# Kernel optimization log

Hardware: AMD Instinct MI355X
Metric: run time of the kernel (lower is better)

Reference implementation:

```python
import jax, jax.numpy as jnp
import numpy as np

T, D = 2048, 2048
H, DN, DR, DV = 16, 128, 64, 128
QL, KVL = 768, 512
HI, DI, TOPK = 16, 128, 256
E, TKE, MI = 8, 2, 1024
EPS = 1e-6
RSF = 2.5
SCALE = (DN + DR) ** -0.5
NEG = jnp.float32(-1e30)


def rms_norm(x, w):
    xf = x.astype(jnp.float32)
    y = xf * jax.lax.rsqrt(jnp.mean(xf * xf, axis=-1, keepdims=True) + EPS)
    return (y * w).astype(x.dtype)


def layer_norm(x, w, b):
    xf = x.astype(jnp.float32)
    mu = jnp.mean(xf, axis=-1, keepdims=True)
    var = jnp.mean((xf - mu) ** 2, axis=-1, keepdims=True)
    return (((xf - mu) * jax.lax.rsqrt(var + EPS)) * w + b).astype(x.dtype)


def rope(x, pos):
    # neox-style half rotation; x: (T, ..., d)
    d = x.shape[-1]
    inv = 1.0 / (10000.0 ** (jnp.arange(0, d, 2, dtype=jnp.float32) / d))
    f = pos.astype(jnp.float32)[:, None] * inv  # (T, d/2)
    shp = (x.shape[0],) + (1,) * (x.ndim - 2) + (d // 2,)
    cos, sin = jnp.cos(f).reshape(shp), jnp.sin(f).reshape(shp)
    x1, x2 = jnp.split(x.astype(jnp.float32), 2, axis=-1)
    return jnp.concatenate([x1 * cos - x2 * sin, x2 * cos + x1 * sin], -1).astype(x.dtype)


def swiglu(x, w1, w3, w2):
    return (jax.nn.silu(x @ w1) * (x @ w3)) @ w2


def setup_inputs():
    key = jax.random.key(0)
    ks = iter(jax.random.split(key, 32))
    n = lambda shape, s=0.02: jax.random.normal(next(ks), shape, jnp.float32) * s
    return dict(
        positions=jnp.arange(T, dtype=jnp.int32),
        hidden_states=jax.random.normal(next(ks), (T, D), jnp.float32),
        w_in=jnp.ones((D,), jnp.float32),
        w_post=jnp.ones((D,), jnp.float32),
        W_qkv_a=n((D, QL + KVL + DR)),
        w_qa=jnp.ones((QL,), jnp.float32),
        w_kva=jnp.ones((KVL,), jnp.float32),
        W_qb=n((QL, H * (DN + DR))),
        W_ik=n((D, DI)),
        ik_ln_w=jnp.ones((DI,), jnp.float32),
        ik_ln_b=jnp.zeros((DI,), jnp.float32),
        W_iw=n((D, HI)),
        W_iqb=n((QL, HI * DI)),
        W_UKT=n((H, DN, KVL)),
        W_UV=n((H, KVL, DV)),
        W_o=n((H * DV, D)),
        W_gate=n((D, E)),
        We1=n((E, D, MI)), We3=n((E, D, MI)), We2=n((E, MI, D)),
        Ws1=n((D, MI)), Ws3=n((D, MI)), Ws2=n((MI, D)),
    )


def reference(positions, hidden_states, w_in, w_post, W_qkv_a, w_qa, w_kva, W_qb,
              W_ik, ik_ln_w, ik_ln_b, W_iw, W_iqb, W_UKT, W_UV, W_o, W_gate,
              We1, We3, We2, Ws1, Ws3, Ws2):
    # --- input norm (residual is None path) ---
    residual = hidden_states
    h = rms_norm(hidden_states, w_in)

    # --- fused qkv_a projection + split ---
    qkv = h @ W_qkv_a
    q_c, kv_c, k_pe = jnp.split(qkv, [QL, QL + KVL], axis=-1)

    # --- lightning indexer projections ---
    index_k = layer_norm(h @ W_ik, ik_ln_w, ik_ln_b)  # (T, DI)
    index_w = (h @ W_iw) * (HI ** -0.5)               # (T, HI)

    # --- fused_norm_rope: q_a/kv_a RMSNorm, RoPE on k_pe and index_k ---
    q_c = rms_norm(q_c, w_qa)
    kv_c = rms_norm(kv_c, w_kva)
    k_pe = rope(k_pe, positions)
    index_k = rope(index_k, positions)

    # --- q_b / indexer q projections + fused_q RoPE ---
    q = (q_c @ W_qb).reshape(T, H, DN + DR)
    q_nope, q_pe = q[..., :DN], rope(q[..., DN:], positions)
    index_q = rope((q_c @ W_iqb).reshape(T, HI, DI), positions) * (DI ** -0.5)

    # --- sparse_attn_indexer: weighted ReLU dot-product logits, causal top-k ---
    il = jnp.einsum('thd,sd->ths', index_q, index_k)
    il = jnp.einsum('ths,th->ts', jax.nn.relu(il), index_w)  # (T, T)
    causal = positions[:, None] >= positions[None, :]
    il = jnp.where(causal, il, NEG)
    topk_idx = jax.lax.top_k(il, TOPK)[1]  # (T, TOPK)
    mask = jnp.zeros((T, T), bool).at[jnp.arange(T)[:, None], topk_idx].set(True) & causal

    # --- MLA sparse decode (MQA in latent space) ---
    ql_nope = jnp.einsum('thd,hdk->thk', q_nope, W_UKT)       # (T, H, KVL)
    q_full = jnp.concatenate([ql_nope, q_pe], axis=-1)        # (T, H, KVL+DR)
    kv = jnp.concatenate([kv_c, k_pe], axis=-1)               # (T, KVL+DR)
    scores = jnp.einsum('thd,sd->ths', q_full, kv) * SCALE
    scores = jnp.where(mask[:, None, :], scores, NEG)
    attn = jax.nn.softmax(scores, axis=-1)
    ctx = jnp.einsum('ths,sk->thk', attn, kv_c)               # (T, H, KVL)
    o = jnp.einsum('thk,hkv->thv', ctx, W_UV).reshape(T, H * DV) @ W_o

    # --- add + post-attention norm ---
    residual = o + residual
    h = rms_norm(residual, w_post)

    # --- MoE: top-2 softmax routing over 8 experts + shared expert ---
    probs = jax.nn.softmax(h @ W_gate, axis=-1)
    tv, ti = jax.lax.top_k(probs, TKE)
    tw = tv / jnp.sum(tv, axis=-1, keepdims=True)
    routed = jnp.zeros_like(h)
    for e in range(E):
        we = jnp.sum(jnp.where(ti == e, tw, 0.0), axis=-1)  # (T,)
        routed = routed + we[:, None] * swiglu(h, We1[e], We3[e], We2[e])
    shared = swiglu(h, Ws1, Ws3, Ws2)
    # scale_and_add in fp32
    out = (routed.astype(jnp.float32) * RSF + shared.astype(jnp.float32)).astype(h.dtype)
    return out, residual
```

## Files before the change

kernel.cpp:

```cpp
#include <hip/hip_runtime.h>
#include <hip/hip_bf16.h>
#include <math.h>

#define TT 2048
#define DD 2048
#define NH 16
#define DNN 128
#define DRR 64
#define DVV 128
#define QLL 768
#define KVLL 512
#define HII 16
#define DII 128
#define TOPKN 256
#define NEE 8
#define MII 1024
#define QKVW 1488
#define QW 5120
#define EPSF 1e-6f
#define NEGF (-1e30f)
#define SCALEF 0.07216878364870323f
#define IQSCALE 0.08838834764831845f
#define LOG1E4 9.210340371976184f
#define CHK 512

typedef unsigned short u16;
typedef __attribute__((ext_vector_type(8))) short s8v;
typedef __attribute__((ext_vector_type(4))) float f4v;

__device__ inline void split_bf16(float x, u16& h, u16& l) {
  __hip_bfloat16 bh_ = __float2bfloat16(x);
  float hf = __bfloat162float(bh_);
  __hip_bfloat16 bl_ = __float2bfloat16(x - hf);
  h = *(u16*)&bh_; l = *(u16*)&bl_;
}
__device__ inline u16 rnd_bf16(float x) {
  __hip_bfloat16 b = __float2bfloat16(x);
  return *(u16*)&b;
}
__device__ inline float b2f(u16 h) { return __uint_as_float(((unsigned)h) << 16); }

__global__ __launch_bounds__(256) void rms_kernel(
    const float* __restrict__ src, int sstride, int width,
    const float* __restrict__ w,
    float* __restrict__ dstf, int dfstride,
    u16* __restrict__ dsthi, u16* __restrict__ dstlo, int dhstride)
{
  int t = blockIdx.x, tid = threadIdx.x;
  const float* x = src + (size_t)t * sstride;
  float ss = 0.f;
  for (int i = tid; i < width; i += 256) { float v = x[i]; ss += v * v; }
  for (int off = 32; off; off >>= 1) ss += __shfl_down(ss, off, 64);
  __shared__ float red[4];
  __shared__ float scale_sh;
  if ((tid & 63) == 0) red[tid >> 6] = ss;
  __syncthreads();
  if (tid == 0) {
    float tot = red[0] + red[1] + red[2] + red[3];
    scale_sh = rsqrtf(tot / (float)width + EPSF);
  }
  __syncthreads();
  float sc2 = scale_sh;
  for (int i = tid; i < width; i += 256) {
    float y = x[i] * sc2 * w[i];
    if (dstf) dstf[(size_t)t * dfstride + i] = y;
    if (dsthi) {
      if (dstlo) {
        u16 h, l; split_bf16(y, h, l);
        dsthi[(size_t)t * dhstride + i] = h;
        dstlo[(size_t)t * dhstride + i] = l;
      } else {
        dsthi[(size_t)t * dhstride + i] = rnd_bf16(y);
      }
    }
  }
}

__global__ __launch_bounds__(256) void res_rms(
    const float* __restrict__ o, const float* __restrict__ hid,
    const float* __restrict__ w,
    float* __restrict__ resid, u16* __restrict__ dhi, u16* __restrict__ dlo)
{
  int t = blockIdx.x, tid = threadIdx.x;
  long base = (long)t * DD;
  float xv[8];
  float ss = 0.f;
#pragma unroll
  for (int j = 0; j < 8; ++j) {
    int i = j * 256 + tid;
    float v = o[base + i] + hid[base + i];
    xv[j] = v; resid[base + i] = v; ss += v * v;
  }
  for (int off = 32; off; off >>= 1) ss += __shfl_down(ss, off, 64);
  __shared__ float red[4];
  __shared__ float scale_sh;
  if ((tid & 63) == 0) red[tid >> 6] = ss;
  __syncthreads();
  if (tid == 0) scale_sh = rsqrtf((red[0] + red[1] + red[2] + red[3]) / (float)DD + EPSF);
  __syncthreads();
  float sc2 = scale_sh;
#pragma unroll
  for (int j = 0; j < 8; ++j) {
    int i = j * 256 + tid;
    float y = xv[j] * sc2 * w[i];
    u16 h, l; split_bf16(y, h, l);
    dhi[base + i] = h; dlo[base + i] = l;
  }
}

__global__ __launch_bounds__(128) void ln_rope_ik(
    const float* __restrict__ src, int sstride,
    const float* __restrict__ w, const float* __restrict__ b,
    const int* __restrict__ pos, u16* __restrict__ dhi, u16* __restrict__ dlo)
{
  int t = blockIdx.x, tid = threadIdx.x;
  __shared__ float rowv[128];
  __shared__ float red[2];
  float v = src[(size_t)t * sstride + tid];
  float s = v;
  for (int off = 32; off; off >>= 1) s += __shfl_down(s, off, 64);
  if ((tid & 63) == 0) red[tid >> 6] = s;
  __syncthreads();
  float mu = (red[0] + red[1]) * (1.f / 128.f);
  __syncthreads();
  float dlt = v - mu;
  float s2 = dlt * dlt;
  for (int off = 32; off; off >>= 1) s2 += __shfl_down(s2, off, 64);
  if ((tid & 63) == 0) red[tid >> 6] = s2;
  __syncthreads();
  float var = (red[0] + red[1]) * (1.f / 128.f);
  float yv = dlt * rsqrtf(var + EPSF) * w[tid] + b[tid];
  rowv[tid] = yv;
  __syncthreads();
  if (tid < 64) {
    float x1 = rowv[tid], x2 = rowv[tid + 64];
    float p = (float)pos[t];
    float invf = expf(-(2.f * tid / 128.f) * LOG1E4);
    float f = p * invf;
    float cf = cosf(f), sf = sinf(f);
    float y1 = x1 * cf - x2 * sf;
    float y2 = x2 * cf + x1 * sf;
    u16 h1, l1, h2, l2;
    split_bf16(y1, h1, l1); split_bf16(y2, h2, l2);
    long base = (size_t)t * DII + tid;
    dhi[base] = h1; dlo[base] = l1;
    dhi[base + 64] = h2; dlo[base + 64] = l2;
  }
}

__global__ void rope_kpe(const float* __restrict__ qkv, const int* __restrict__ pos, u16* __restrict__ kvb)
{
  int t = blockIdx.x, tid = threadIdx.x;
  if (tid < 32) {
    const float* x = qkv + (size_t)t * QKVW + QLL + KVLL;
    float x1 = x[tid], x2 = x[tid + 32];
    float p = (float)pos[t];
    float invf = expf(-(2.f * tid / 64.f) * LOG1E4);
    float f = p * invf, cf = cosf(f), sf = sinf(f);
    kvb[(long)t * 576 + 512 + tid]      = rnd_bf16(x1 * cf - x2 * sf);
    kvb[(long)t * 576 + 512 + tid + 32] = rnd_bf16(x2 * cf + x1 * sf);
  }
}

__global__ void rope_qpe(float* __restrict__ q, const int* __restrict__ pos)
{
  int t = blockIdx.x, tid = threadIdx.x;
  int h = tid >> 5, j = tid & 31;
  float* x = q + (size_t)t * QW + h * 192 + 128;
  float x1 = x[j], x2 = x[j + 32];
  float p = (float)pos[t];
  float invf = expf(-(2.f * j / 64.f) * LOG1E4);
  float f = p * invf, cf = cosf(f), sf = sinf(f);
  x[j]      = x1 * cf - x2 * sf;
  x[j + 32] = x2 * cf + x1 * sf;
}

__global__ __launch_bounds__(256) void rope_iq_cvt(
    const float* __restrict__ q, const int* __restrict__ pos,
    u16* __restrict__ dhi, u16* __restrict__ dlo)
{
  int t = blockIdx.x, tid = threadIdx.x;
  float p = (float)pos[t];
#pragma unroll
  for (int r = 0; r < 4; ++r) {
    int e = r * 256 + tid;
    int h = e >> 6, j = e & 63;
    long src = (long)t * QW + 3072 + h * 128 + j;
    long dst = (long)t * 2048 + h * 128 + j;
    float x1 = q[src], x2 = q[src + 64];
    float invf = expf(-(2.f * j / 128.f) * LOG1E4);
    float f = p * invf, cf = cosf(f), sf = sinf(f);
    float y1 = (x1 * cf - x2 * sf) * IQSCALE;
    float y2 = (x2 * cf + x1 * sf) * IQSCALE;
    u16 h1, l1, h2, l2;
    split_bf16(y1, h1, l1); split_bf16(y2, h2, l2);
    dhi[dst] = h1; dlo[dst] = l1;
    dhi[dst + 64] = h2; dlo[dst + 64] = l2;
  }
}

__global__ __launch_bounds__(256) void cvt_qnope(
    const float* __restrict__ q, u16* __restrict__ hi, u16* __restrict__ lo)
{
  int t = blockIdx.x;
  int e = threadIdx.x * 8;
  int h = e >> 7, d = e & 127;
  const float* src = q + (long)t * QW + h * 192 + d;
  float4 a = *(const float4*)src;
  float4 b = *(const float4*)(src + 4);
  ushort4 h0, l0, h1, l1;
  split_bf16(a.x, h0.x, l0.x); split_bf16(a.y, h0.y, l0.y);
  split_bf16(a.z, h0.z, l0.z); split_bf16(a.w, h0.w, l0.w);
  split_bf16(b.x, h1.x, l1.x); split_bf16(b.y, h1.y, l1.y);
  split_bf16(b.z, h1.z, l1.z); split_bf16(b.w, h1.w, l1.w);
  long ob = (long)t * 2048 + e;
  *(ushort4*)(hi + ob) = h0; *(ushort4*)(hi + ob + 4) = h1;
  *(ushort4*)(lo + ob) = l0; *(ushort4*)(lo + ob + 4) = l1;
}

__global__ __launch_bounds__(256) void cvt_wT(
    const float* __restrict__ W, u16* __restrict__ hiT, u16* __restrict__ loT, int K, int N)
{
  int z = blockIdx.z;
  const float* in = W + (long)z * K * N;
  u16* ho = hiT + (long)z * K * N;
  u16* lo2 = loT ? loT + (long)z * K * N : nullptr;
  int k0 = blockIdx.y * 32, n0 = blockIdx.x * 32;
  __shared__ float tile[32][33];
  int r = threadIdx.x >> 3, c4 = (threadIdx.x & 7) * 4;
  float4 v = *(const float4*)(in + (long)(k0 + r) * N + n0 + c4);
  tile[r][c4] = v.x; tile[r][c4 + 1] = v.y; tile[r][c4 + 2] = v.z; tile[r][c4 + 3] = v.w;
  __syncthreads();
  float a0 = tile[c4 + 0][r], a1 = tile[c4 + 1][r], a2 = tile[c4 + 2][r], a3 = tile[c4 + 3][r];
  ushort4 h, l;
  split_bf16(a0, h.x, l.x);
  split_bf16(a1, h.y, l.y);
  split_bf16(a2, h.z, l.z);
  split_bf16(a3, h.w, l.w);
  long ob = (long)(n0 + r) * K + k0 + c4;
  *(ushort4*)(ho + ob) = h;
  if (lo2) *(ushort4*)(lo2 + ob) = l;
}

__global__ void cvt_wT_small(const float* __restrict__ W, u16* __restrict__ hiT, u16* __restrict__ loT,
                             int K, int N, float scale)
{
  int i = blockIdx.x * 256 + threadIdx.x;
  if (i >= K * N) return;
  int n = i / K, k = i - n * K;
  float v = W[(long)k * N + n] * scale;
  u16 h, l; split_bf16(v, h, l);
  hiT[i] = h; loT[i] = l;
}

template<int TERMS, int OUTMODE, int KS = 1>
__global__ __launch_bounds__(256) void gemm_bx2(
    const u16* __restrict__ Ahi, const u16* __restrict__ Alo, int lda, long astride,
    const u16* __restrict__ BThi, const u16* __restrict__ BTlo, long bstride,
    float* __restrict__ C, u16* __restrict__ Chi, u16* __restrict__ Clo, int ldc, long cstride,
    int M, int N, int K,
    const int* __restrict__ rowlist, const int* __restrict__ offs, const int* __restrict__ cnts,
    const int* __restrict__ crows, const float* __restrict__ cw)
{
  int zz = blockIdx.z;
  int ksp = (KS > 1) ? (zz % KS) : 0;
  int z = (KS > 1) ? (zz / KS) : zz;
  Ahi += (long)z * astride;
  BThi += (long)z * bstride;
  if (TERMS == 3) { Alo += (long)z * astride; BTlo += (long)z * bstride; }
  if (OUTMODE == 1) { Chi += (long)z * cstride; Clo += (long)z * cstride; }
  else { C += (long)z * cstride; }
  int moff = 0, Mloc = M;
  if (offs) { moff = offs[z]; Mloc = cnts[z]; }
  int m0 = blockIdx.y * 128;
  if (m0 >= Mloc) return;
  int n0 = blockIdx.x * 128;
  int tid = threadIdx.x;

  __shared__ u16 Ah[128][40];
  __shared__ u16 Bh[128][40];
  __shared__ u16 Al[TERMS == 3 ? 128 : 1][40];
  __shared__ u16 Bl[TERMS == 3 ? 128 : 1][40];

  int r0 = tid >> 2, c0 = (tid & 3) * 8;
  int r1 = 64 + r0, c1 = c0;

  long aoff0 = -1, aoff1 = -1;
  {
    int g0 = moff + m0 + r0;
    int g1 = moff + m0 + r1;
    if (m0 + r0 < Mloc) aoff0 = (long)(rowlist ? rowlist[g0] : g0) * lda;
    if (m0 + r1 < Mloc) aoff1 = (long)(rowlist ? rowlist[g1] : g1) * lda;
  }
  long boff0 = (n0 + r0 < N) ? (long)(n0 + r0) * K : -1;
  long boff1 = (n0 + r1 < N) ? (long)(n0 + r1) * K : -1;

  f4v acc[4][4];
#pragma unroll
  for (int i = 0; i < 4; ++i)
#pragma unroll
    for (int j = 0; j < 4; ++j) acc[i][j] = (f4v){0.f, 0.f, 0.f, 0.f};

  int wid = tid >> 6, lane = tid & 63;
  int wr = wid >> 1, wc = wid & 1;
  int frow = lane & 15, koct = (lane >> 4) * 8;

  int kbeg = (KS > 1) ? (K / KS) * ksp : 0;
  int kend = (KS > 1) ? kbeg + K / KS : K;
  for (int kt = kbeg; kt < kend; kt += 32) {
    uint4 zzv = make_uint4(0, 0, 0, 0);
    uint4 ah0 = zzv, ah1 = zzv, bh0 = zzv, bh1 = zzv;
    uint4 al0 = zzv, al1 = zzv, bl0 = zzv, bl1 = zzv;
    if (aoff0 >= 0) ah0 = *(const uint4*)(Ahi + aoff0 + kt + c0);
    if (aoff1 >= 0) ah1 = *(const uint4*)(Ahi + aoff1 + kt + c1);
    if (boff0 >= 0) bh0 = *(const uint4*)(BThi + boff0 + kt + c0);
    if (boff1 >= 0) bh1 = *(const uint4*)(BThi + boff1 + kt + c1);
    if (TERMS == 3) {
      if (aoff0 >= 0) al0 = *(const uint4*)(Alo + aoff0 + kt + c0);
      if (aoff1 >= 0) al1 = *(const uint4*)(Alo + aoff1 + kt + c1);
      if (boff0 >= 0) bl0 = *(const uint4*)(BTlo + boff0 + kt + c0);
      if (boff1 >= 0) bl1 = *(const uint4*)(BTlo + boff1 + kt + c1);
    }
    __syncthreads();
    *(uint4*)&Ah[r0][c0] = ah0;
    *(uint4*)&Ah[r1][c1] = ah1;
    *(uint4*)&Bh[r0][c0] = bh0;
    *(uint4*)&Bh[r1][c1] = bh1;
    if (TERMS == 3) {
      *(uint4*)&Al[r0][c0] = al0;
      *(uint4*)&Al[r1][c1] = al1;
      *(uint4*)&Bl[r0][c0] = bl0;
      *(uint4*)&Bl[r1][c1] = bl1;
    }
    __syncthreads();

    s8v af_h[4], af_l[4];
#pragma unroll
    for (int i = 0; i < 4; ++i) {
      af_h[i] = *(const s8v*)&Ah[wr * 64 + i * 16 + frow][koct];
      if (TERMS == 3) af_l[i] = *(const s8v*)&Al[wr * 64 + i * 16 + frow][koct];
    }
#pragma unroll
    for (int j = 0; j < 4; ++j) {
      s8v bf_h = *(const s8v*)&Bh[wc * 64 + j * 16 + frow][koct];
      s8v bf_l;
      if (TERMS == 3) bf_l = *(const s8v*)&Bl[wc * 64 + j * 16 + frow][koct];
#pragma unroll
      for (int i = 0; i < 4; ++i) {
        acc[i][j] = __builtin_amdgcn_mfma_f32_16x16x32_bf16(af_h[i], bf_h, acc[i][j], 0, 0, 0);
        if (TERMS == 3) {
          acc[i][j] = __builtin_amdgcn_mfma_f32_16x16x32_bf16(af_h[i], bf_l, acc[i][j], 0, 0, 0);
          acc[i][j] = __builtin_amdgcn_mfma_f32_16x16x32_bf16(af_l[i], bf_h, acc[i][j], 0, 0, 0);
        }
      }
    }
  }

#pragma unroll
  for (int i = 0; i < 4; ++i) {
    int gmb = m0 + wr * 64 + i * 16 + (lane >> 4) * 4;
#pragma unroll
    for (int j = 0; j < 4; ++j) {
      int gn = n0 + wc * 64 + j * 16 + (lane & 15);
      if (gn >= N) continue;
#pragma unroll
      for (int r = 0; r < 4; ++r) {
        int gm = gmb + r;
        if (gm >= Mloc) continue;
        float v = acc[i][j][r];
        long cidx = (long)(moff + gm) * ldc + gn;
        if (OUTMODE == 0) {
          if (KS > 1) atomicAdd(&C[cidx], v);
          else C[cidx] = v;
        } else if (OUTMODE == 1) {
          u16 hh, ll; split_bf16(v, hh, ll);
          Chi[cidx] = hh; Clo[cidx] = ll;
        } else {
          int tr = crows[moff + gm];
          atomicAdd(&C[(long)tr * ldc + gn], cw[moff + gm] * v);
        }
      }
    }
  }
}

__global__ __launch_bounds__(256) void index_score_mfma(
    const u16* __restrict__ iqhi, const u16* __restrict__ iqlo,
    const u16* __restrict__ ikhi, const u16* __restrict__ iklo,
    const float* __restrict__ iww, int iws, float* __restrict__ ts)
{
  int s0 = blockIdx.x * 64, t0 = blockIdx.y * 64;
  int tid = threadIdx.x;
  if (s0 > t0 + 63) {
    for (int r = 0; r < 16; ++r) {
      int lin = r * 256 + tid;
      int i = lin >> 6, j = lin & 63;
      ts[(size_t)(t0 + i) * TT + s0 + j] = NEGF;
    }
    return;
  }
  __shared__ u16 Ah[64][128];
  __shared__ u16 Al[64][128];
  __shared__ u16 Bh[64][128];
  __shared__ u16 Bl[64][128];

  for (int it = tid; it < 1024; it += 256) {
    int r = it >> 4, c = it & 15;
    int cs = (c ^ (r & 7)) * 8;
    *(uint4*)&Bh[r][cs] = *(const uint4*)(ikhi + (size_t)(s0 + r) * 128 + c * 8);
    *(uint4*)&Bl[r][cs] = *(const uint4*)(iklo + (size_t)(s0 + r) * 128 + c * 8);
  }

  int wid = tid >> 6, lane = tid & 63;
  int wr = wid >> 1, wc = wid & 1;
  int frow = lane & 15, kq = lane >> 4;

  f4v accts[2][2];
#pragma unroll
  for (int i = 0; i < 2; ++i)
#pragma unroll
    for (int j = 0; j < 2; ++j) accts[i][j] = (f4v){0.f, 0.f, 0.f, 0.f};

  for (int h = 0; h < 16; ++h) {
    __syncthreads();
    const u16* iqh_p = iqhi + (size_t)t0 * 2048 + h * 128;
    const u16* iql_p = iqlo + (size_t)t0 * 2048 + h * 128;
    for (int it = tid; it < 1024; it += 256) {
      int r = it >> 4, c = it & 15;
      int cs = (c ^ (r & 7)) * 8;
      *(uint4*)&Ah[r][cs] = *(const uint4*)(iqh_p + (size_t)r * 2048 + c * 8);
      *(uint4*)&Al[r][cs] = *(const uint4*)(iql_p + (size_t)r * 2048 + c * 8);
    }
    __syncthreads();
    f4v acch[2][2];
#pragma unroll
    for (int i = 0; i < 2; ++i)
#pragma unroll
      for (int j = 0; j < 2; ++j) acch[i][j] = (f4v){0.f, 0.f, 0.f, 0.f};
#pragma unroll
    for (int ks = 0; ks < 4; ++ks) {
      s8v ah[2], al[2], bh[2], bl[2];
#pragma unroll
      for (int i = 0; i < 2; ++i) {
        int rr = wr * 32 + i * 16 + frow;
        int cb = ((ks * 4 + kq) ^ (rr & 7)) * 8;
        ah[i] = *(const s8v*)&Ah[rr][cb];
        al[i] = *(const s8v*)&Al[rr][cb];
      }
#pragma unroll
      for (int j = 0; j < 2; ++j) {
        int rr = wc * 32 + j * 16 + frow;
        int cb = ((ks * 4 + kq) ^ (rr & 7)) * 8;
        bh[j] = *(const s8v*)&Bh[rr][cb];
        bl[j] = *(const s8v*)&Bl[rr][cb];
      }
#pragma unroll
      for (int i = 0; i < 2; ++i)
#pragma unroll
        for (int j = 0; j < 2; ++j) {
          acch[i][j] = __builtin_amdgcn_mfma_f32_16x16x32_bf16(ah[i], bh[j], acch[i][j], 0, 0, 0);
          acch[i][j] = __builtin_amdgcn_mfma_f32_16x16x32_bf16(ah[i], bl[j], acch[i][j], 0, 0, 0);
          acch[i][j] = __builtin_amdgcn_mfma_f32_16x16x32_bf16(al[i], bh[j], acch[i][j], 0, 0, 0);
        }
    }
#pragma unroll
    for (int i = 0; i < 2; ++i) {
#pragma unroll
      for (int r = 0; r < 4; ++r) {
        int tl = wr * 32 + i * 16 + kq * 4 + r;
        float wv = iww[(size_t)(t0 + tl) * iws + h];
#pragma unroll
        for (int j = 0; j < 2; ++j)
          accts[i][j][r] += fmaxf(acch[i][j][r], 0.f) * wv;
      }
    }
  }
#pragma unroll
  for (int i = 0; i < 2; ++i) {
#pragma unroll
    for (int j = 0; j < 2; ++j) {
      int ssb = s0 + wc * 32 + j * 16 + frow;
#pragma unroll
      for (int r = 0; r < 4; ++r) {
        int tt = t0 + wr * 32 + i * 16 + kq * 4 + r;
        ts[(size_t)tt * TT + ssb] = (ssb <= tt) ? accts[i][j][r] : NEGF;
      }
    }
  }
}

__global__ __launch_bounds__(256) void topk_kernel(
    const float* __restrict__ ts, int* __restrict__ sel_idx, int* __restrict__ sel_cnt)
{
  int t = blockIdx.x, tid = threadIdx.x;
  __shared__ unsigned keys[2048];
  __shared__ int hist[256];
  __shared__ int scan[256];
  __shared__ int sh_b, sh_r, sh_G;
  const float* row = ts + (size_t)t * TT;
  for (int i = tid; i < 2048; i += 256) {
    unsigned u = __float_as_uint(row[i]);
    keys[i] = (u & 0x80000000u) ? ~u : (u | 0x80000000u);
  }
  if (tid == 0) { sh_r = TOPKN; sh_G = 0; }
  unsigned prefix = 0, pmask = 0;
  __syncthreads();
  for (int lvl = 0; lvl < 4; ++lvl) {
    int sh = 24 - lvl * 8;
    hist[tid] = 0;
    __syncthreads();
    for (int i = tid; i < 2048; i += 256) {
      unsigned k = keys[i];
      if ((k & pmask) == prefix) atomicAdd(&hist[(k >> sh) & 255], 1);
    }
    __syncthreads();
    if (tid == 0) {
      int r = sh_r, G = sh_G;
      int b = 255;
      for (;; --b) {
        int c = hist[b];
        if (c >= r) break;
        r -= c; G += c;
      }
      sh_b = b; sh_r = r; sh_G = G;
    }
    __syncthreads();
    prefix |= ((unsigned)sh_b) << sh;
    pmask |= 0xFFu << sh;
    __syncthreads();
  }
  unsigned kth = prefix;
  int G = sh_G;
  int R = TOPKN - G;
  int base = tid * 8;
  int ceq = 0;
  for (int c = 0; c < 8; ++c) ceq += (keys[base + c] == kth);
  scan[tid] = ceq;
  __syncthreads();
  for (int off = 1; off < 256; off <<= 1) {
    int add = (tid >= off) ? scan[tid - off] : 0;
    __syncthreads();
    scan[tid] += add;
    __syncthreads();
  }
  int eqb = scan[tid] - ceq;
  unsigned flags = 0; int nsel = 0, eqrun = 0;
  for (int c = 0; c < 8; ++c) {
    int s = base + c; unsigned k = keys[s];
    bool sel = (k > kth) || ((k == kth) && (eqb + eqrun < R));
    eqrun += (k == kth);
    sel = sel && (s <= t);
    if (sel) { flags |= 1u << c; ++nsel; }
  }
  __syncthreads();
  scan[tid] = nsel;
  __syncthreads();
  for (int off = 1; off < 256; off <<= 1) {
    int add = (tid >= off) ? scan[tid - off] : 0;
    __syncthreads();
    scan[tid] += add;
    __syncthreads();
  }
  int wbase = scan[tid] - nsel;
  int k2 = 0;
  for (int c = 0; c < 8; ++c)
    if (flags & (1u << c)) { sel_idx[(size_t)t * TOPKN + wbase + k2] = base + c; ++k2; }
  if (tid == 255) sel_cnt[t] = scan[255];
}

#define SM_TILE 0
#define SM_QH   74752
#define SM_QL   93440
#define SM_S    112128
#define SM_SIDX 128768
#define SM_INVD 129792
#define SM_TOT  129856
__global__ __launch_bounds__(256) void attn_mfma(
    const u16* __restrict__ qlfhi, const u16* __restrict__ qlflo,
    const float* __restrict__ q, int tbase,
    const u16* __restrict__ kvb,
    const int* __restrict__ sel_idx, const int* __restrict__ sel_cnt,
    u16* __restrict__ ctxhi, u16* __restrict__ ctxlo)
{
  extern __shared__ char smem[];
  u16* tA = (u16*)(smem + SM_TILE);
  u16* tT = (u16*)(smem + SM_TILE);
  u16* qh = (u16*)(smem + SM_QH);
  u16* ql = (u16*)(smem + SM_QL);
  float* S = (float*)(smem + SM_S);
  int* sidx = (int*)(smem + SM_SIDX);
  float* invd = (float*)(smem + SM_INVD);

  int lt = blockIdx.x, tid = threadIdx.x;
  int t = tbase + lt;
  int lane = tid & 63, w = tid >> 6;
  int frow = lane & 15, kq = lane >> 4;
  int cnt = sel_cnt[t];

  if (tid < 256) sidx[tid] = (tid < cnt) ? sel_idx[(long)t * TOPKN + tid] : 0;
  for (int u = tid; u < 16 * 72; u += 256) {
    int h = u / 72, dg = u % 72; int d = dg * 8;
    if (d < 512) {
      uint4 vh = *(const uint4*)(qlfhi + (long)lt * 8192 + h * 512 + d);
      uint4 vl = *(const uint4*)(qlflo + (long)lt * 8192 + h * 512 + d);
      *(uint4*)(qh + h * 584 + d) = vh;
      *(uint4*)(ql + h * 584 + d) = vl;
    } else {
      const float* src = q + (long)t * QW + h * 192 + 128 + (d - 512);
      float4 a = *(const float4*)src;
      float4 b = *(const float4*)(src + 4);
      float pv[8] = {a.x, a.y, a.z, a.w, b.x, b.y, b.z, b.w};
      u16 hh[8], ll[8];
#pragma unroll
      for (int j = 0; j < 8; ++j) split_bf16(pv[j], hh[j], ll[j]);
#pragma unroll
      for (int j = 0; j < 8; ++j) { qh[h * 584 + d + j] = hh[j]; ql[h * 584 + d + j] = ll[j]; }
    }
  }
  __syncthreads();
  for (int tile = 0; tile < 4; ++tile) {
    for (int u = tid; u < 64 * 72; u += 256) {
      int dg = u % 72, s = u / 72;
      int key = sidx[tile * 64 + s];
      uint4 v = *(const uint4*)(kvb + (long)key * 576 + dg * 8);
      *(uint4*)(tA + s * 584 + dg * 8) = v;
    }
    __syncthreads();
    f4v acc = (f4v){0.f, 0.f, 0.f, 0.f};
#pragma unroll
    for (int ks = 0; ks < 18; ++ks) {
      s8v a_h = *(const s8v*)(qh + frow * 584 + ks * 32 + kq * 8);
      s8v a_l = *(const s8v*)(ql + frow * 584 + ks * 32 + kq * 8);
      s8v b   = *(const s8v*)(tA + (w * 16 + frow) * 584 + ks * 32 + kq * 8);
      acc = __builtin_amdgcn_mfma_f32_16x16x32_bf16(a_h, b, acc, 0, 0, 0);
      acc = __builtin_amdgcn_mfma_f32_16x16x32_bf16(a_l, b, acc, 0, 0, 0);
    }
#pragma unroll
    for (int r = 0; r < 4; ++r)
      S[(kq * 4 + r) * 260 + tile * 64 + w * 16 + frow] = acc[r] * SCALEF;
    __syncthreads();
  }
  {
    int h = tid >> 4, l = tid & 15;
    float m = -INFINITY;
    for (int i = l; i < 256; i += 16) if (i < cnt) m = fmaxf(m, S[h * 260 + i]);
    for (int off2 = 8; off2; off2 >>= 1) m = fmaxf(m, __shfl_xor(m, off2, 16));
    float ssum = 0.f;
    for (int i = l; i < 256; i += 16) {
      float e = (i < cnt) ? expf(S[h * 260 + i] - m) : 0.f;
      S[h * 260 + i] = e; ssum += e;
    }
    for (int off2 = 8; off2; off2 >>= 1) ssum += __shfl_xor(ssum, off2, 16);
    if (l == 0) invd[h] = 1.f / ssum;
  }
  __syncthreads();
  f4v cacc[8];
#pragma unroll
  for (int nt = 0; nt < 8; ++nt) cacc[nt] = (f4v){0.f, 0.f, 0.f, 0.f};
  for (int tile = 0; tile < 4; ++tile) {
    for (int u = tid; u < 64 * 64; u += 256) {
      int s = u & 63, dg = u >> 6;
      int key = sidx[tile * 64 + s];
      uint4 v = *(const uint4*)(kvb + (long)key * 576 + dg * 8);
      u16 tmp[8]; *(uint4*)tmp = v;
#pragma unroll
      for (int j = 0; j < 8; ++j) tT[(dg * 8 + j) * 72 + s] = tmp[j];
    }
    __syncthreads();
#pragma unroll
    for (int ks = 0; ks < 2; ++ks) {
      float4 p0 = *(const float4*)(S + frow * 260 + tile * 64 + ks * 32 + kq * 8);
      float4 p1 = *(const float4*)(S + frow * 260 + tile * 64 + ks * 32 + kq * 8 + 4);
      float pv[8] = {p0.x, p0.y, p0.z, p0.w, p1.x, p1.y, p1.z, p1.w};
      union { s8v v; u16 u[8]; } pah, pal;
#pragma unroll
      for (int j = 0; j < 8; ++j) split_bf16(pv[j], pah.u[j], pal.u[j]);
#pragma unroll
      for (int nt = 0; nt < 8; ++nt) {
        s8v b = *(const s8v*)(tT + (w * 128 + nt * 16 + frow) * 72 + ks * 32 + kq * 8);
        cacc[nt] = __builtin_amdgcn_mfma_f32_16x16x32_bf16(pah.v, b, cacc[nt], 0, 0, 0);
        cacc[nt] = __builtin_amdgcn_mfma_f32_16x16x32_bf16(pal.v, b, cacc[nt], 0, 0, 0);
      }
    }
    __syncthreads();
  }
#pragma unroll
  for (int nt = 0; nt < 8; ++nt) {
    int dim = w * 128 + nt * 16 + frow;
#pragma unroll
    for (int r = 0; r < 4; ++r) {
      int head = kq * 4 + r;
      float v = cacc[nt][r] * invd[head];
      u16 hh, ll; split_bf16(v, hh, ll);
      long ob = (long)lt * 8192 + head * 512 + dim;
      ctxhi[ob] = hh; ctxlo[ob] = ll;
    }
  }
}

__global__ void silu_cvt(const float* __restrict__ u, const float* __restrict__ v,
                         u16* __restrict__ outhi, long n)
{
  long i = ((long)blockIdx.x * 256 + threadIdx.x) * 4;
  if (i >= n) return;
  float4 a = *(const float4*)(u + i);
  float4 b = *(const float4*)(v + i);
  ushort4 h;
  h.x = rnd_bf16(a.x / (1.f + expf(-a.x)) * b.x);
  h.y = rnd_bf16(a.y / (1.f + expf(-a.y)) * b.y);
  h.z = rnd_bf16(a.z / (1.f + expf(-a.z)) * b.z);
  h.w = rnd_bf16(a.w / (1.f + expf(-a.w)) * b.w);
  *(ushort4*)(outhi + i) = h;
}

__global__ void zero_counts(int* cnt, int* cursor)
{ int i = threadIdx.x; if (i < 8) { cnt[i] = 0; cursor[i] = 0; } }

__global__ void gate_pick(const float* __restrict__ glog,
                          int* __restrict__ e01, float* __restrict__ w01, int* __restrict__ cnt)
{
  int t = blockIdx.x * 256 + threadIdx.x;
  if (t >= TT) return;
  float lg[8];
#pragma unroll
  for (int i = 0; i < 8; ++i) lg[i] = glog[(long)t * 8 + i];
  float m = lg[0];
#pragma unroll
  for (int i = 1; i < 8; ++i) m = fmaxf(m, lg[i]);
  float pe[8];
#pragma unroll
  for (int i = 0; i < 8; ++i) pe[i] = expf(lg[i] - m);
  int i0 = 0;
  for (int i = 1; i < 8; ++i) if (pe[i] > pe[i0]) i0 = i;
  int i1 = (i0 == 0) ? 1 : 0;
  for (int i = 0; i < 8; ++i) if (i != i0 && pe[i] > pe[i1]) i1 = i;
  float w0 = pe[i0], w1v = pe[i1];
  float invs = 1.f / (w0 + w1v);
  e01[2 * t] = i0; e01[2 * t + 1] = i1;
  w01[2 * t] = w0 * invs; w01[2 * t + 1] = w1v * invs;
  atomicAdd(&cnt[i0], 1); atomicAdd(&cnt[i1], 1);
}

__global__ void offsets_kernel(const int* cnt, int* offs)
{
  if (threadIdx.x == 0) {
    int a = 0;
    for (int e = 0; e < 8; ++e) { offs[e] = a; a += cnt[e]; }
    offs[8] = a;
  }
}

__global__ void build_list(const int* __restrict__ e01, const float* __restrict__ w01,
                           const int* __restrict__ offs, int* __restrict__ cursor,
                           int* __restrict__ list_tok, float* __restrict__ wlist)
{
  int t = blockIdx.x * 256 + threadIdx.x;
  if (t >= TT) return;
  for (int k = 0; k < 2; ++k) {
    int e = e01[2 * t + k];
    int p2 = atomicAdd(&cursor[e], 1);
    int g = offs[e] + p2;
    list_tok[g] = t;
    wlist[g] = w01[2 * t + k] * 2.5f;
  }
}

extern "C" void kernel_launch(void* const* d_in, const int* in_sizes, int n_in,
                              void* d_out, int out_size, void* d_ws, size_t ws_size,
                              hipStream_t stream)
{
  (void)in_sizes; (void)n_in; (void)out_size; (void)ws_size;
  const int*   positions = (const int*)d_in[0];
  const float* hidden    = (const float*)d_in[1];
  const float* w_in      = (const float*)d_in[2];
  const float* w_post    = (const float*)d_in[3];
  const float* W_qkv_a   = (const float*)d_in[4];
  const float* w_qa      = (const float*)d_in[5];
  const float* w_kva     = (const float*)d_in[6];
  const float* W_qb      = (const float*)d_in[7];
  const float* W_ik      = (const float*)d_in[8];
  const float* ik_ln_w   = (const float*)d_in[9];
  const float* ik_ln_b   = (const float*)d_in[10];
  const float* W_iw      = (const float*)d_in[11];
  const float* W_iqb     = (const float*)d_in[12];
  const float* W_UKT     = (const float*)d_in[13];
  const float* W_UV      = (const float*)d_in[14];
  const float* W_o       = (const float*)d_in[15];
  const float* W_gate    = (const float*)d_in[16];
  const float* We1       = (const float*)d_in[17];
  const float* We3       = (const float*)d_in[18];
  const float* We2       = (const float*)d_in[19];
  const float* Ws1       = (const float*)d_in[20];
  const float* Ws3       = (const float*)d_in[21];
  const float* Ws2       = (const float*)d_in[22];

  float* outp  = (float*)d_out;
  float* resid = outp + (size_t)TT * DD;

  float* ws = (float*)d_ws;
  size_t o = 0;
  auto take = [&](size_t n) { float* p = ws + o; o += n; return p; };
  float* kvbF  = take(589824);
  float* reg1  = take(4325376);
  float* qcF   = take(1572864);
  float* bikF  = take(262144);
  float* biw   = take(32768);
  float* bq    = take(6291456);
  float* biq   = take(4194304);
  float* bts   = take(4194304);
  float* wshiF = take(4194304);
  float* wsloF = take(2097152);
  u16*   hhi   = (u16*)take(2097152);
  u16*   hlo   = (u16*)take(2097152);
  int*   bsel  = (int*)take(524288);
  int*   bselc = (int*)take(2048);
  int*   be01  = (int*)take(4096);
  float* bw01  = take(4096);
  int*   bcnt  = (int*)take(16);
  int*   boff  = (int*)take(16);
  int*   bcur  = (int*)take(16);
  int*   blist = (int*)take(4096);
  float* bwlist= take(4096);

  u16*   kvb   = (u16*)kvbF;
  float* bqkvx = reg1;
  u16*   qnhi  = (u16*)reg1;
  u16*   qnlo  = qnhi + 4194304;
  u16*   qchi  = (u16*)qcF;
  u16*   qclo  = qchi + 1572864;
  u16*   ikhi  = (u16*)bikF;
  u16*   iklo  = ikhi + 262144;
  float* qfull = bq;
  u16*   iqhi  = (u16*)wshiF;
  u16*   iqlo  = iqhi + 4194304;
  u16*   qlfhi = (u16*)bts;
  u16*   qlflo = (u16*)(bts + 2097152);
  u16*   ctxhi = (u16*)wshiF;
  u16*   ctxlo = (u16*)(wshiF + 2097152);
  u16*   bahi  = hhi;
  u16*   balo  = hlo;
  float* bo    = bts;
  u16*   ushi  = (u16*)bts;
  float* glog  = biw;
  u16*   wshi  = (u16*)wshiF;
  u16*   wslo  = (u16*)wsloF;
  u16*   wukthi = (u16*)wsloF;
  u16*   wuktlo = wukthi + 1048576;
  u16*   wuvhi  = wukthi + 2097152;
  u16*   wuvlo  = wukthi + 3145728;
  float* bu    = bq;
  u16*   uhi   = (u16*)(bq + 4194304);
  float* us    = biq;
  float* vs    = biq + 2097152;
  float* bv    = kvbF;

  const int* NOI = nullptr; const float* NOF = nullptr;
  u16* NOU = nullptr;
  float* NOFP = nullptr;

  hipMemsetAsync(bqkvx, 0, (size_t)TT * QKVW * 4, stream);
  rms_kernel<<<TT, 256, 0, stream>>>(hidden, DD, DD, w_in, NOFP, 0, hhi, hlo, DD);
  cvt_wT<<<dim3(1344 / 32, DD / 32, 1), 256, 0, stream>>>(W_qkv_a, wshi, wslo, DD, 1344);
  cvt_wT<<<dim3(DII / 32, DD / 32, 1), 256, 0, stream>>>(W_ik, wshi + (long)1344 * DD, wslo + (long)1344 * DD, DD, DII);
  cvt_wT_small<<<(HII * DD + 255) / 256, 256, 0, stream>>>(W_iw, wshi + (long)1472 * DD, wslo + (long)1472 * DD, DD, HII, 0.25f);
  gemm_bx2<3, 0, 2><<<dim3(12, 16, 2), 256, 0, stream>>>(
      hhi, hlo, DD, 0, wshi, wslo, 0, bqkvx, NOU, NOU, QKVW, 0,
      TT, QKVW, DD, NOI, NOI, NOI, NOI, NOF);
  rms_kernel<<<TT, 256, 0, stream>>>(bqkvx, QKVW, QLL, w_qa, NOFP, 0, qchi, qclo, QLL);
  rms_kernel<<<TT, 256, 0, stream>>>(bqkvx + QLL, QKVW, KVLL, w_kva, NOFP, 0, kvb, NOU, 576);
  rope_kpe<<<TT, 64, 0, stream>>>(bqkvx, positions, kvb);
  ln_rope_ik<<<TT, 128, 0, stream>>>(bqkvx + 1344, QKVW, ik_ln_w, ik_ln_b, positions, ikhi, iklo);
  cvt_wT<<<dim3(3072 / 32, QLL / 32, 1), 256, 0, stream>>>(W_qb, wshi, wslo, QLL, 3072);
  cvt_wT<<<dim3(2048 / 32, QLL / 32, 1), 256, 0, stream>>>(W_iqb, wshi + (long)3072 * QLL, wslo + (long)3072 * QLL, QLL, 2048);
  gemm_bx2<3, 0><<<dim3(40, 16, 1), 256, 0, stream>>>(
      qchi, qclo, QLL, 0, wshi, wslo, 0, qfull, NOU, NOU, QW, 0,
      TT, QW, QLL, NOI, NOI, NOI, NOI, NOF);
  rope_iq_cvt<<<TT, 256, 0, stream>>>(qfull, positions, iqhi, iqlo);
  index_score_mfma<<<dim3(32, 32, 1), 256, 0, stream>>>(iqhi, iqlo, ikhi, iklo, bqkvx + 1472, QKVW, bts);
  topk_kernel<<<TT, 256, 0, stream>>>(bts, bsel, bselc);
  rope_qpe<<<TT, 512, 0, stream>>>(qfull, positions);
  cvt_qnope<<<TT, 256, 0, stream>>>(qfull, qnhi, qnlo);
  cvt_wT<<<dim3(KVLL / 32, DNN / 32, NH), 256, 0, stream>>>(W_UKT, wukthi, wuktlo, DNN, KVLL);
  cvt_wT<<<dim3(DVV / 32, KVLL / 32, NH), 256, 0, stream>>>(W_UV, wuvhi, wuvlo, KVLL, DVV);
  for (int c = 0; c < TT / CHK; ++c) {
    int base = c * CHK;
    gemm_bx2<3, 1><<<dim3(4, CHK / 128, NH), 256, 0, stream>>>(
        qnhi + (long)base * 2048, qnlo + (long)base * 2048, 2048, 128,
        wukthi, wuktlo, (long)KVLL * DNN,
        nullptr, qlfhi, qlflo, NH * KVLL, KVLL,
        CHK, KVLL, DNN, NOI, NOI, NOI, NOI, NOF);
    attn_mfma<<<CHK, 256, SM_TOT, stream>>>(qlfhi, qlflo, qfull, base, kvb, bsel, bselc, ctxhi, ctxlo);
    gemm_bx2<3, 1><<<dim3(1, CHK / 128, NH), 256, 0, stream>>>(
        ctxhi, ctxlo, NH * KVLL, KVLL,
        wuvhi, wuvlo, (long)DVV * KVLL,
        nullptr, bahi + (long)base * DD, balo + (long)base * DD, DD, DVV,
        CHK, DVV, KVLL, NOI, NOI, NOI, NOI, NOF);
  }
  hipMemsetAsync(bo, 0, (size_t)TT * DD * 4, stream);
  cvt_wT<<<dim3(DD / 32, DD / 32, 1), 256, 0, stream>>>(W_o, wshi, wslo, DD, DD);
  gemm_bx2<3, 0, 2><<<dim3(16, 16, 2), 256, 0, stream>>>(
      bahi, balo, DD, 0, wshi, wslo, 0, bo, NOU, NOU, DD, 0,
      TT, DD, DD, NOI, NOI, NOI, NOI, NOF);
  res_rms<<<TT, 256, 0, stream>>>(bo, hidden, w_post, resid, hhi, hlo);
  zero_counts<<<1, 64, 0, stream>>>(bcnt, bcur);
  hipMemsetAsync(glog, 0, (size_t)TT * NEE * 4, stream);
  cvt_wT_small<<<(NEE * DD + 255) / 256, 256, 0, stream>>>(W_gate, wshi, wslo, DD, NEE, 1.0f);
  gemm_bx2<3, 0, 2><<<dim3(1, 16, 2), 256, 0, stream>>>(
      hhi, hlo, DD, 0, wshi, wslo, 0, glog, NOU, NOU, NEE, 0,
      TT, NEE, DD, NOI, NOI, NOI, NOI, NOF);
  gate_pick<<<TT / 256, 256, 0, stream>>>(glog, be01, bw01, bcnt);
  offsets_kernel<<<1, 64, 0, stream>>>(bcnt, boff);
  build_list<<<TT / 256, 256, 0, stream>>>(be01, bw01, boff, bcur, blist, bwlist);
  hipMemsetAsync(us, 0, (size_t)2 * TT * MII * 4, stream);
  cvt_wT<<<dim3(MII / 32, DD / 32, 1), 256, 0, stream>>>(Ws1, wshi, NOU, DD, MII);
  gemm_bx2<1, 0, 2><<<dim3(8, 16, 2), 256, 0, stream>>>(
      hhi, NOU, DD, 0, wshi, NOU, 0, us, NOU, NOU, MII, 0,
      TT, MII, DD, NOI, NOI, NOI, NOI, NOF);
  cvt_wT<<<dim3(MII / 32, DD / 32, 1), 256, 0, stream>>>(Ws3, wshi, NOU, DD, MII);
  gemm_bx2<1, 0, 2><<<dim3(8, 16, 2), 256, 0, stream>>>(
      hhi, NOU, DD, 0, wshi, NOU, 0, vs, NOU, NOU, MII, 0,
      TT, MII, DD, NOI, NOI, NOI, NOI, NOF);
  silu_cvt<<<(TT * MII) / 1024, 256, 0, stream>>>(us, vs, ushi, (long)TT * MII);
  cvt_wT<<<dim3(DD / 32, MII / 32, 1), 256, 0, stream>>>(Ws2, wshi, NOU, MII, DD);
  gemm_bx2<1, 0><<<dim3(16, 16, 1), 256, 0, stream>>>(
      ushi, NOU, MII, 0, wshi, NOU, 0, outp, NOU, NOU, DD, 0,
      TT, DD, MII, NOI, NOI, NOI, NOI, NOF);
  for (int hf = 0; hf < 2; ++hf) {
    const float* w1p = We1 + (size_t)hf * 4 * DD * MII;
    cvt_wT<<<dim3(MII / 32, DD / 32, 4), 256, 0, stream>>>(w1p, wshi, NOU, DD, MII);
    gemm_bx2<1, 0><<<dim3(8, 16, 4), 256, 0, stream>>>(
        hhi, NOU, DD, 0, wshi, NOU, (long)DD * MII, bu, NOU, NOU, MII, 0,
        0, MII, DD, blist, boff + 4 * hf, bcnt + 4 * hf, NOI, NOF);
  }
  for (int hf = 0; hf < 2; ++hf) {
    const float* w3p = We3 + (size_t)hf * 4 * DD * MII;
    cvt_wT<<<dim3(MII / 32, DD / 32, 4), 256, 0, stream>>>(w3p, wshi, NOU, DD, MII);
    gemm_bx2<1, 0><<<dim3(8, 16, 4), 256, 0, stream>>>(
        hhi, NOU, DD, 0, wshi, NOU, (long)DD * MII, bv, NOU, NOU, MII, 0,
        0, MII, DD, blist, boff + 4 * hf, bcnt + 4 * hf, NOI, NOF);
  }
  silu_cvt<<<(2 * TT * MII) / 1024, 256, 0, stream>>>(bu, bv, uhi, (long)2 * TT * MII);
  for (int hf = 0; hf < 2; ++hf) {
    const float* w2p = We2 + (size_t)hf * 4 * MII * DD;
    cvt_wT<<<dim3(DD / 32, MII / 32, 4), 256, 0, stream>>>(w2p, wshi, NOU, MII, DD);
    gemm_bx2<1, 2><<<dim3(16, 16, 4), 256, 0, stream>>>(
        uhi, NOU, MII, 0, wshi, NOU, (long)MII * DD, outp, NOU, NOU, DD, 0,
        0, DD, MII, NOI, boff + 4 * hf, bcnt + 4 * hf, blist, bwlist);
  }
}
```

Baseline: 1.580 ms.

## Double attn_mfma block to 512 threads with split-K score accumulation

The sparse attention kernel now runs 512 threads per block. In the QK^T phase, two groups of four waves each handle half of the 576-wide reduction and write partial scores to separate LDS buffers, which the softmax sums and scales. In the PV phase, each wave covers 64 output dims instead of 128. The aim is more parallel MFMA work per token and half the accumulator registers per wave, at the cost of extra LDS (about 146 KB), which may limit blocks per CU.

```diff
diff --git a/kernel.cpp b/kernel.cpp
--- a/kernel.cpp
+++ b/kernel.cpp
@@ -572,10 +572,11 @@
 #define SM_QH   74752
 #define SM_QL   93440
 #define SM_S    112128
-#define SM_SIDX 128768
-#define SM_INVD 129792
-#define SM_TOT  129856
-__global__ __launch_bounds__(256) void attn_mfma(
+#define SM_S2   128768
+#define SM_SIDX 145408
+#define SM_INVD 146432
+#define SM_TOT  146496
+__global__ __launch_bounds__(512) void attn_mfma(
     const u16* __restrict__ qlfhi, const u16* __restrict__ qlflo,
     const float* __restrict__ q, int tbase,
     const u16* __restrict__ kvb,
@@ -587,7 +588,8 @@
   u16* tT = (u16*)(smem + SM_TILE);
   u16* qh = (u16*)(smem + SM_QH);
   u16* ql = (u16*)(smem + SM_QL);
-  float* S = (float*)(smem + SM_S);
+  float* S1 = (float*)(smem + SM_S);
+  float* S2 = (float*)(smem + SM_S2);
   int* sidx = (int*)(smem + SM_SIDX);
   float* invd = (float*)(smem + SM_INVD);
 
@@ -595,10 +597,12 @@
   int t = tbase + lt;
   int lane = tid & 63, w = tid >> 6;
   int frow = lane & 15, kq = lane >> 4;
+  int wk = w >> 2;
+  int wn = w & 3;
   int cnt = sel_cnt[t];
 
   if (tid < 256) sidx[tid] = (tid < cnt) ? sel_idx[(long)t * TOPKN + tid] : 0;
-  for (int u = tid; u < 16 * 72; u += 256) {
+  for (int u = tid; u < 16 * 72; u += 512) {
     int h = u / 72, dg = u % 72; int d = dg * 8;
     if (d < 512) {
       uint4 vh = *(const uint4*)(qlfhi + (long)lt * 8192 + h * 512 + d);
@@ -619,7 +623,9 @@
   }
   __syncthreads();
   for (int tile = 0; tile < 4; ++tile) {
-    for (int u = tid; u < 64 * 72; u += 256) {
+#pragma unroll
+    for (int it = 0; it < 9; ++it) {
+      int u = tid + it * 512;
       int dg = u % 72, s = u / 72;
       int key = sidx[tile * 64 + s];
       uint4 v = *(const uint4*)(kvb + (long)key * 576 + dg * 8);
@@ -628,37 +634,43 @@
     __syncthreads();
     f4v acc = (f4v){0.f, 0.f, 0.f, 0.f};
 #pragma unroll
-    for (int ks = 0; ks < 18; ++ks) {
+    for (int ki = 0; ki < 9; ++ki) {
+      int ks = wk * 9 + ki;
       s8v a_h = *(const s8v*)(qh + frow * 584 + ks * 32 + kq * 8);
       s8v a_l = *(const s8v*)(ql + frow * 584 + ks * 32 + kq * 8);
-      s8v b   = *(const s8v*)(tA + (w * 16 + frow) * 584 + ks * 32 + kq * 8);
+      s8v b   = *(const s8v*)(tA + (wn * 16 + frow) * 584 + ks * 32 + kq * 8);
       acc = __builtin_amdgcn_mfma_f32_16x16x32_bf16(a_h, b, acc, 0, 0, 0);
       acc = __builtin_amdgcn_mfma_f32_16x16x32_bf16(a_l, b, acc, 0, 0, 0);
     }
+    float* Sd = wk ? S2 : S1;
 #pragma unroll
     for (int r = 0; r < 4; ++r)
-      S[(kq * 4 + r) * 260 + tile * 64 + w * 16 + frow] = acc[r] * SCALEF;
+      Sd[(kq * 4 + r) * 260 + tile * 64 + wn * 16 + frow] = acc[r];
     __syncthreads();
   }
   {
-    int h = tid >> 4, l = tid & 15;
+    int h = tid >> 5, l = tid & 31;
     float m = -INFINITY;
-    for (int i = l; i < 256; i += 16) if (i < cnt) m = fmaxf(m, S[h * 260 + i]);
-    for (int off2 = 8; off2; off2 >>= 1) m = fmaxf(m, __shfl_xor(m, off2, 16));
+    for (int i = l; i < 256; i += 32)
+      if (i < cnt) m = fmaxf(m, (S1[h * 260 + i] + S2[h * 260 + i]) * SCALEF);
+    for (int off2 = 16; off2; off2 >>= 1) m = fmaxf(m, __shfl_xor(m, off2, 32));
     float ssum = 0.f;
-    for (int i = l; i < 256; i += 16) {
-      float e = (i < cnt) ? expf(S[h * 260 + i] - m) : 0.f;
-      S[h * 260 + i] = e; ssum += e;
-    }
-    for (int off2 = 8; off2; off2 >>= 1) ssum += __shfl_xor(ssum, off2, 16);
+    for (int i = l; i < 256; i += 32) {
+      float sv = (S1[h * 260 + i] + S2[h * 260 + i]) * SCALEF;
+      float e = (i < cnt) ? expf(sv - m) : 0.f;
+      S1[h * 260 + i] = e; ssum += e;
+    }
+    for (int off2 = 16; off2; off2 >>= 1) ssum += __shfl_xor(ssum, off2, 32);
     if (l == 0) invd[h] = 1.f / ssum;
   }
   __syncthreads();
-  f4v cacc[8];
-#pragma unroll
-  for (int nt = 0; nt < 8; ++nt) cacc[nt] = (f4v){0.f, 0.f, 0.f, 0.f};
+  f4v cacc[4];
+#pragma unroll
+  for (int nt = 0; nt < 4; ++nt) cacc[nt] = (f4v){0.f, 0.f, 0.f, 0.f};
   for (int tile = 0; tile < 4; ++tile) {
-    for (int u = tid; u < 64 * 64; u += 256) {
+#pragma unroll
+    for (int it = 0; it < 8; ++it) {
+      int u = tid + it * 512;
       int s = u & 63, dg = u >> 6;
       int key = sidx[tile * 64 + s];
       uint4 v = *(const uint4*)(kvb + (long)key * 576 + dg * 8);
@@ -669,15 +681,15 @@
     __syncthreads();
 #pragma unroll
     for (int ks = 0; ks < 2; ++ks) {
-      float4 p0 = *(const float4*)(S + frow * 260 + tile * 64 + ks * 32 + kq * 8);
-      float4 p1 = *(const float4*)(S + frow * 260 + tile * 64 + ks * 32 + kq * 8 + 4);
+      float4 p0 = *(const float4*)(S1 + frow * 260 + tile * 64 + ks * 32 + kq * 8);
+      float4 p1 = *(const float4*)(S1 + frow * 260 + tile * 64 + ks * 32 + kq * 8 + 4);
       float pv[8] = {p0.x, p0.y, p0.z, p0.w, p1.x, p1.y, p1.z, p1.w};
       union { s8v v; u16 u[8]; } pah, pal;
 #pragma unroll
       for (int j = 0; j < 8; ++j) split_bf16(pv[j], pah.u[j], pal.u[j]);
 #pragma unroll
-      for (int nt = 0; nt < 8; ++nt) {
-        s8v b = *(const s8v*)(tT + (w * 128 + nt * 16 + frow) * 72 + ks * 32 + kq * 8);
+      for (int nt = 0; nt < 4; ++nt) {
+        s8v b = *(const s8v*)(tT + (w * 64 + nt * 16 + frow) * 72 + ks * 32 + kq * 8);
         cacc[nt] = __builtin_amdgcn_mfma_f32_16x16x32_bf16(pah.v, b, cacc[nt], 0, 0, 0);
         cacc[nt] = __builtin_amdgcn_mfma_f32_16x16x32_bf16(pal.v, b, cacc[nt], 0, 0, 0);
       }
@@ -685,8 +697,8 @@
     __syncthreads();
   }
 #pragma unroll
-  for (int nt = 0; nt < 8; ++nt) {
-    int dim = w * 128 + nt * 16 + frow;
+  for (int nt = 0; nt < 4; ++nt) {
+    int dim = w * 64 + nt * 16 + frow;
 #pragma unroll
     for (int r = 0; r < 4; ++r) {
       int head = kq * 4 + r;
@@ -889,7 +901,7 @@
         wukthi, wuktlo, (long)KVLL * DNN,
         nullptr, qlfhi, qlflo, NH * KVLL, KVLL,
         CHK, KVLL, DNN, NOI, NOI, NOI, NOI, NOF);
-    attn_mfma<<<CHK, 256, SM_TOT, stream>>>(qlfhi, qlflo, qfull, base, kvb, bsel, bselc, ctxhi, ctxlo);
+    attn_mfma<<<CHK, 512, SM_TOT, stream>>>(qlfhi, qlflo, qfull, base, kvb, bsel, bselc, ctxhi, ctxlo);
     gemm_bx2<3, 1><<<dim3(1, CHK / 128, NH), 256, 0, stream>>>(
         ctxhi, ctxlo, NH * KVLL, KVLL,
         wuvhi, wuvlo, (long)DVV * KVLL,
```

After: 1.476 ms. 1.07x faster.
